# Optimization experiments

Hardware: AMD Instinct MI355X
Metric: run time of the kernel (lower is better)

The kernel has to match this reference:

```python
import jax, jax.numpy as jnp
import numpy as np
import math

WS = 11
SIGMA = 1.5

def _gaussian_window(ws=WS, sigma=SIGMA):
    i = np.arange(ws)
    g = np.exp(-((i - ws // 2) ** 2) / (2.0 * sigma ** 2))
    g = (g / g.sum()).astype(np.float32)
    w2d = np.outer(g, g)  # [ws, ws]
    return jnp.asarray(w2d)

def _depthwise_conv(x, win2d):
    # x: [B, C, H, W]; win2d: [ws, ws]
    C = x.shape[1]
    kernel = jnp.broadcast_to(win2d[None, None], (C, 1, WS, WS)).astype(x.dtype)  # [C,1,ws,ws]
    return jax.lax.conv_general_dilated(
        x, kernel,
        window_strides=(1, 1),
        padding=[(WS // 2, WS // 2), (WS // 2, WS // 2)],
        dimension_numbers=("NCHW", "OIHW", "NCHW"),
        feature_group_count=C,
    )

def setup_inputs() -> dict:
    key = jax.random.key(0)
    k1, k2, k3 = jax.random.split(key, 3)
    B, C, H, W = 16, 3, 512, 512
    x = jax.random.uniform(k1, (B, C, H, W), dtype=jnp.float32)
    y = jax.random.uniform(k2, (B, C, H, W), dtype=jnp.float32)
    conf = jax.random.uniform(k3, (B, 1, H, W), dtype=jnp.float32)
    return {"x": x, "y": y, "conf": conf}

def reference(x, y, conf):
    win2d = _gaussian_window()
    mu_x = _depthwise_conv(x, win2d)
    mu_y = _depthwise_conv(y, win2d)
    mu_x2, mu_y2, mu_xy = mu_x * mu_x, mu_y * mu_y, mu_x * mu_y
    sigma_x2 = _depthwise_conv(x * x, win2d) - mu_x2
    sigma_y2 = _depthwise_conv(y * y, win2d) - mu_y2
    sigma_xy = _depthwise_conv(x * y, win2d) - mu_xy
    C1, C2 = 0.01 ** 2, 0.03 ** 2
    ssim = (2 * mu_xy + C1) * (2 * sigma_xy + C2) / ((mu_x2 + mu_y2 + C1) * (sigma_x2 + sigma_y2 + C2))
    loss_map = jnp.clip(1.0 - ssim, 0.0, 1.0)
    loss_map = loss_map * conf  # broadcast over channels
    return jnp.mean(loss_map)
```

## Files before the change

### kernel.cpp

```cpp
#include <hip/hip_runtime.h>
#include <cmath>

#define TW 32
#define TH 48
#define HR (TH + 10)
#define IMG 512
#define SSIM_C1 1e-4f
#define SSIM_C2 9e-4f

struct GaussWin { float g[11]; };

typedef float v2f __attribute__((ext_vector_type(2)));

__device__ __forceinline__ v2f pk_fma(v2f a, v2f b, v2f c) {
    return __builtin_elementwise_fma(a, b, c);
}
__device__ __forceinline__ v2f pk_mul(v2f a, v2f b) { return a * b; }

__launch_bounds__(256, 4)
__global__ void ssim_tile_kernel(const float* __restrict__ x,
                                 const float* __restrict__ y,
                                 const float* __restrict__ conf,
                                 float* __restrict__ partials,
                                 float* __restrict__ out,
                                 int use_ws, float scale,
                                 GaussWin W) {
    __shared__ float4 s_h4[HR * TW];
    __shared__ float  s_h1[HR * TW];
    __shared__ float  s_red[4];

    const int tid = threadIdx.x;
    const int plane = blockIdx.z;
    const int tx0 = blockIdx.x * TW;
    const int ty0 = blockIdx.y * TH;
    const int pbase = plane * (IMG * IMG);
    const int cbase = (plane / 3) * (IMG * IMG);

    constexpr int WI[11] = {0,1,2,3,4,5,4,3,2,1,0};
    v2f w2[6];
    #pragma unroll
    for (int i = 0; i < 6; i++) w2[i] = (v2f){W.g[i], W.g[i]};

    const bool interior = (blockIdx.x >= 1) & (blockIdx.x <= 14) &
                          (blockIdx.y >= 1) & (blockIdx.y <= 9);

    if (tid < HR * 4) {
        const int r = tid >> 2;
        const int cs = (tid & 3) * 8;
        const int gy = ty0 - 5 + r;
        const float* xrow = x + pbase + gy * IMG;
        const float* yrow = y + pbase + gy * IMG;
        const int c0 = tx0 + cs - 8;

        float4 fx[6], fy[6];
        if (interior) {
            #pragma unroll
            for (int q = 0; q < 6; q++) {
                fx[q] = *(const float4*)(xrow + c0 + 4 * q);
                fy[q] = *(const float4*)(yrow + c0 + 4 * q);
            }
        } else {
            const bool rowok = ((unsigned)gy < IMG);
            #pragma unroll
            for (int q = 0; q < 6; q++) {
                int col = c0 + 4 * q;
                fx[q] = make_float4(0.f, 0.f, 0.f, 0.f);
                fy[q] = make_float4(0.f, 0.f, 0.f, 0.f);
                if (rowok && (unsigned)col <= (unsigned)(IMG - 4)) {
                    fx[q] = *(const float4*)(xrow + col);
                    fy[q] = *(const float4*)(yrow + col);
                }
            }
        }
        float vxa[24], vya[24];
        #pragma unroll
        for (int q = 0; q < 6; q++) {
            vxa[4*q+0]=fx[q].x; vxa[4*q+1]=fx[q].y; vxa[4*q+2]=fx[q].z; vxa[4*q+3]=fx[q].w;
            vya[4*q+0]=fy[q].x; vya[4*q+1]=fy[q].y; vya[4*q+2]=fy[q].z; vya[4*q+3]=fy[q].w;
        }

        v2f amu[8], as2[8];
        float axy[8];
        #pragma unroll
        for (int j = 0; j < 8; j++) { amu[j]=(v2f){0.f,0.f}; as2[j]=(v2f){0.f,0.f}; axy[j]=0.f; }
        #pragma unroll
        for (int k = 0; k < 18; k++) {
            float xv = vxa[k + 3], yv = vya[k + 3];
            v2f xy = (v2f){xv, yv};
            v2f p2 = pk_mul(xy, xy);
            float pxy = xv * yv;
            const int jlo = (k - 10 > 0) ? (k - 10) : 0;
            const int jhi = (k < 7) ? k : 7;
            #pragma unroll
            for (int j = jlo; j <= jhi; j++) {
                v2f w = w2[WI[k - j]];
                amu[j] = pk_fma(xy, w, amu[j]);
                as2[j] = pk_fma(p2, w, as2[j]);
                axy[j] = fmaf(pxy, w.x, axy[j]);
            }
        }
        const int quad = cs & 24;
        const int base0 = cs + 2 * (cs >> 3) + 5 * r;
        #pragma unroll
        for (int j = 0; j < 8; j++) {
            int pc = quad | ((base0 + j) & 7);
            s_h4[r * TW + pc] = make_float4(amu[j].x, amu[j].y, as2[j].x, as2[j].y);
            s_h1[r * TW + pc] = axy[j];
        }
    }

    const int c  = tid & 31;
    const int r0 = (tid >> 5) * 6;
    float cf[6];
    #pragma unroll
    for (int j = 0; j < 6; j++) {
        int gy = ty0 + r0 + j;
        cf[j] = (gy < IMG) ? conf[cbase + gy * IMG + tx0 + c] : 0.f;
    }
    __syncthreads();

    v2f amu[6], as2[6];
    float axy[6];
    #pragma unroll
    for (int j = 0; j < 6; j++) { amu[j]=(v2f){0.f,0.f}; as2[j]=(v2f){0.f,0.f}; axy[j]=0.f; }

    const int cquad = c & 24;
    const int cb0 = c + 2 * (c >> 3) + 5 * r0;
    #pragma unroll
    for (int t = 0; t < 16; t++) {
        int row = r0 + t;
        int pc = cquad | ((cb0 + 5 * t) & 7);
        float4 h4 = s_h4[row * TW + pc];
        float  h1 = s_h1[row * TW + pc];
        v2f hmu = (v2f){h4.x, h4.y};
        v2f hs2 = (v2f){h4.z, h4.w};
        #pragma unroll
        for (int j = 0; j < 6; j++) {
            int k = t - j;
            if (k >= 0 && k <= 10) {
                v2f w = w2[WI[k]];
                amu[j] = pk_fma(hmu, w, amu[j]);
                as2[j] = pk_fma(hs2, w, as2[j]);
                axy[j] = fmaf(h1, w.x, axy[j]);
            }
        }
    }

    float lsum = 0.f;
    #pragma unroll
    for (int j = 0; j < 6; j++) {
        float mu_x = amu[j].x, mu_y = amu[j].y;
        float mu_x2 = mu_x * mu_x;
        float mu_y2 = mu_y * mu_y;
        float mu_xy = mu_x * mu_y;
        float sigx  = as2[j].x - mu_x2;
        float sigy  = as2[j].y - mu_y2;
        float sigxy = axy[j] - mu_xy;
        float num = (2.f * mu_xy + SSIM_C1) * (2.f * sigxy + SSIM_C2);
        float den = (mu_x2 + mu_y2 + SSIM_C1) * (sigx + sigy + SSIM_C2);
        float ssim = num * __builtin_amdgcn_rcpf(den);
        float loss = 1.f - ssim;
        loss = fminf(fmaxf(loss, 0.f), 1.f);
        lsum = fmaf(loss, cf[j], lsum);
    }

    #pragma unroll
    for (int off = 32; off; off >>= 1) lsum += __shfl_down(lsum, off, 64);
    if ((tid & 63) == 0) s_red[tid >> 6] = lsum;
    __syncthreads();
    if (tid == 0) {
        float t = s_red[0] + s_red[1] + s_red[2] + s_red[3];
        if (use_ws) {
            partials[blockIdx.x + gridDim.x * (blockIdx.y + gridDim.y * blockIdx.z)] = t;
        } else {
            atomicAdd(out, t * scale);
        }
    }
}

__global__ void reduce_kernel(const float* __restrict__ partials, int n,
                              float* __restrict__ out, float scale) {
    __shared__ float s_red[16];
    float s = 0.f;
    const float4* p4 = (const float4*)partials;
    const int n4 = n >> 2;
    for (int i = threadIdx.x; i < n4; i += 1024) {
        float4 v = p4[i];
        s += (v.x + v.y) + (v.z + v.w);
    }
    for (int i = (n4 << 2) + threadIdx.x; i < n; i += 1024) s += partials[i];
    #pragma unroll
    for (int off = 32; off; off >>= 1) s += __shfl_down(s, off, 64);
    if ((threadIdx.x & 63) == 0) s_red[threadIdx.x >> 6] = s;
    __syncthreads();
    if (threadIdx.x == 0) {
        float t = 0.f;
        #pragma unroll
        for (int i = 0; i < 16; i++) t += s_red[i];
        out[0] = t * scale;
    }
}

extern "C" void kernel_launch(void* const* d_in, const int* in_sizes, int n_in,
                              void* d_out, int out_size, void* d_ws, size_t ws_size,
                              hipStream_t stream) {
    const float* x    = (const float*)d_in[0];
    const float* y    = (const float*)d_in[1];
    const float* conf = (const float*)d_in[2];
    float* out = (float*)d_out;
    float* partials = (float*)d_ws;

    GaussWin W;
    {
        double gd[11], s = 0.0;
        for (int i = 0; i < 11; i++) { gd[i] = exp(-((i - 5) * (i - 5)) / 4.5); s += gd[i]; }
        for (int i = 0; i < 11; i++) W.g[i] = (float)(gd[i] / s);
    }

    const int B = 16, C = 3;
    const float scale = 1.0f / (float)(B * C * IMG * IMG);
    const int gy_blocks = (IMG + TH - 1) / TH;
    dim3 grid(IMG / TW, gy_blocks, B * C);
    const int nblocks = (IMG / TW) * gy_blocks * B * C;
    const int use_ws = (ws_size >= (size_t)nblocks * sizeof(float)) ? 1 : 0;

    if (!use_ws) {
        hipMemsetAsync(d_out, 0, sizeof(float), stream);
    }
    ssim_tile_kernel<<<grid, 256, 0, stream>>>(x, y, conf, partials, out, use_ws, scale, W);
    if (use_ws) {
        reduce_kernel<<<1, 1024, 0, stream>>>(partials, nblocks, out, scale);
    }
}
```

Baseline: 160.7 us.

## Shrink tile height to 32, raise occupancy, pack cross-term vertical pass

Tile height drops from 48 to 32 rows so the grid divides the image evenly, which removes the wasted last row-tile and the conf bounds check. The minimum-waves hint in launch bounds goes from 4 to 6 to allow more resident blocks per CU. In the vertical pass the x*y cross-term is accumulated two output rows at a time with packed FMAs over shifted weight pairs, and the epilogue uses packed multiplies. The cost is more halo overhead per output row (42 loaded rows for 32 outputs instead of 58 for 48) and tighter register limits.

Result: slower. 164.5 us (+2.4%).

```diff
diff --git a/kernel.cpp b/kernel.cpp
--- a/kernel.cpp
+++ b/kernel.cpp
@@ -2,7 +2,7 @@
 #include <cmath>
 
 #define TW 32
-#define TH 48
+#define TH 32
 #define HR (TH + 10)
 #define IMG 512
 #define SSIM_C1 1e-4f
@@ -17,7 +17,7 @@
 }
 __device__ __forceinline__ v2f pk_mul(v2f a, v2f b) { return a * b; }
 
-__launch_bounds__(256, 4)
+__launch_bounds__(256, 6)
 __global__ void ssim_tile_kernel(const float* __restrict__ x,
                                  const float* __restrict__ y,
                                  const float* __restrict__ conf,
@@ -42,7 +42,7 @@
     for (int i = 0; i < 6; i++) w2[i] = (v2f){W.g[i], W.g[i]};
 
     const bool interior = (blockIdx.x >= 1) & (blockIdx.x <= 14) &
-                          (blockIdx.y >= 1) & (blockIdx.y <= 9);
+                          (blockIdx.y >= 1) & (blockIdx.y <= 14);
 
     if (tid < HR * 4) {
         const int r = tid >> 2;
@@ -110,24 +110,32 @@
     }
 
     const int c  = tid & 31;
-    const int r0 = (tid >> 5) * 6;
-    float cf[6];
-    #pragma unroll
-    for (int j = 0; j < 6; j++) {
-        int gy = ty0 + r0 + j;
-        cf[j] = (gy < IMG) ? conf[cbase + gy * IMG + tx0 + c] : 0.f;
+    const int r0 = (tid >> 5) * 4;
+    float cf[4];
+    #pragma unroll
+    for (int j = 0; j < 4; j++) {
+        cf[j] = conf[cbase + (ty0 + r0 + j) * IMG + tx0 + c];
     }
     __syncthreads();
 
-    v2f amu[6], as2[6];
-    float axy[6];
-    #pragma unroll
-    for (int j = 0; j < 6; j++) { amu[j]=(v2f){0.f,0.f}; as2[j]=(v2f){0.f,0.f}; axy[j]=0.f; }
+    float ge[12];
+    #pragma unroll
+    for (int i = 0; i < 11; i++) ge[i] = W.g[WI[i]];
+    ge[11] = 0.f;
+    v2f wp[12];
+    #pragma unroll
+    for (int d = 0; d < 12; d++) wp[d] = (v2f){ ge[d], (d == 0) ? 0.f : ge[d - 1] };
+
+    v2f amu[4], as2[4], axy2[2];
+    #pragma unroll
+    for (int j = 0; j < 4; j++) { amu[j]=(v2f){0.f,0.f}; as2[j]=(v2f){0.f,0.f}; }
+    axy2[0] = (v2f){0.f, 0.f};
+    axy2[1] = (v2f){0.f, 0.f};
 
     const int cquad = c & 24;
     const int cb0 = c + 2 * (c >> 3) + 5 * r0;
     #pragma unroll
-    for (int t = 0; t < 16; t++) {
+    for (int t = 0; t < 14; t++) {
         int row = r0 + t;
         int pc = cquad | ((cb0 + 5 * t) & 7);
         float4 h4 = s_h4[row * TW + pc];
@@ -135,32 +143,37 @@
         v2f hmu = (v2f){h4.x, h4.y};
         v2f hs2 = (v2f){h4.z, h4.w};
         #pragma unroll
-        for (int j = 0; j < 6; j++) {
+        for (int j = 0; j < 4; j++) {
             int k = t - j;
             if (k >= 0 && k <= 10) {
                 v2f w = w2[WI[k]];
                 amu[j] = pk_fma(hmu, w, amu[j]);
                 as2[j] = pk_fma(hs2, w, as2[j]);
-                axy[j] = fmaf(h1, w.x, axy[j]);
+            }
+        }
+        v2f h1b = (v2f){h1, h1};
+        #pragma unroll
+        for (int p = 0; p < 2; p++) {
+            int d = t - 2 * p;
+            if (d >= 0 && d <= 11) {
+                axy2[p] = pk_fma(h1b, wp[d], axy2[p]);
             }
         }
     }
 
     float lsum = 0.f;
     #pragma unroll
-    for (int j = 0; j < 6; j++) {
+    for (int j = 0; j < 4; j++) {
         float mu_x = amu[j].x, mu_y = amu[j].y;
-        float mu_x2 = mu_x * mu_x;
-        float mu_y2 = mu_y * mu_y;
+        float axyj = (j & 1) ? axy2[j >> 1].y : axy2[j >> 1].x;
+        v2f prod = pk_mul(amu[j], amu[j]);
         float mu_xy = mu_x * mu_y;
-        float sigx  = as2[j].x - mu_x2;
-        float sigy  = as2[j].y - mu_y2;
-        float sigxy = axy[j] - mu_xy;
-        float num = (2.f * mu_xy + SSIM_C1) * (2.f * sigxy + SSIM_C2);
-        float den = (mu_x2 + mu_y2 + SSIM_C1) * (sigx + sigy + SSIM_C2);
+        v2f sig = as2[j] - prod;
+        float sigxy = axyj - mu_xy;
+        float num = fmaf(2.f, mu_xy, SSIM_C1) * fmaf(2.f, sigxy, SSIM_C2);
+        float den = (prod.x + prod.y + SSIM_C1) * (sig.x + sig.y + SSIM_C2);
         float ssim = num * __builtin_amdgcn_rcpf(den);
-        float loss = 1.f - ssim;
-        loss = fminf(fmaxf(loss, 0.f), 1.f);
+        float loss = fminf(fmaxf(1.f - ssim, 0.f), 1.f);
         lsum = fmaf(loss, cf[j], lsum);
     }
 
@@ -219,9 +232,8 @@
 
     const int B = 16, C = 3;
     const float scale = 1.0f / (float)(B * C * IMG * IMG);
-    const int gy_blocks = (IMG + TH - 1) / TH;
-    dim3 grid(IMG / TW, gy_blocks, B * C);
-    const int nblocks = (IMG / TW) * gy_blocks * B * C;
+    dim3 grid(IMG / TW, IMG / TH, B * C);
+    const int nblocks = (IMG / TW) * (IMG / TH) * B * C;
     const int use_ws = (ws_size >= (size_t)nblocks * sizeof(float)) ? 1 : 0;
 
     if (!use_ws) {
```
